# Kernel tuning notes

Hardware: AMD Instinct MI355X
Metric: run time of the kernel (lower is better)

Reference implementation:

```python
import jax, jax.numpy as jnp
import numpy as np
import math

B, S, D = 4, 1024, 1024
H, DK, DV = 16, 64, 64
MAX_REL = 32  # use_neg_dist=True -> vocab = 2*MAX_REL+1


def setup_inputs() -> dict:
    key = jax.random.key(0)
    ks = jax.random.split(key, 13)
    sc = 0.02
    return {
        "key": jax.random.normal(ks[0], (B, S, D), jnp.float32),
        "value": jax.random.normal(ks[1], (B, S, D), jnp.float32),
        "query": jax.random.normal(ks[2], (B, S, D), jnp.float32),
        "Wk": jax.random.normal(ks[3], (D, H * DK), jnp.float32) * sc,
        "bk": jnp.zeros((H * DK,), jnp.float32),
        "Wq": jax.random.normal(ks[4], (D, H * DK), jnp.float32) * sc,
        "bq": jnp.zeros((H * DK,), jnp.float32),
        "Wv": jax.random.normal(ks[5], (D, H * DV), jnp.float32) * sc,
        "bv": jnp.zeros((H * DV,), jnp.float32),
        "Wo": jax.random.normal(ks[6], (H * DV, D), jnp.float32) * sc,
        "bo": jnp.zeros((D,), jnp.float32),
        "emb_k": jax.random.normal(ks[7], (2 * MAX_REL + 1, DK), jnp.float32) * sc,
        "emb_v": jax.random.normal(ks[8], (2 * MAX_REL + 1, DV), jnp.float32) * sc,
    }


def reference(key, value, query, Wk, bk, Wq, bq, Wv, bv, Wo, bo, emb_k, emb_v):
    # project and split heads -> [B, H, S, d]
    def shape(x, d):
        return x.reshape(B, S, H, d).transpose(0, 2, 1, 3)

    k = shape(key @ Wk + bk, DK)
    v = shape(value @ Wv + bv, DV)
    q = shape(query @ Wq + bq, DK)

    # relative position ids: [S, S] in [0, 2*MAX_REL]
    r = jnp.arange(S)
    rel_idx = jnp.clip(r[None, :] - r[:, None], -MAX_REL, MAX_REL) + MAX_REL
    rel_k = emb_k[rel_idx]  # [S, S, DK]
    rel_v = emb_v[rel_idx]  # [S, S, DV]

    q = q / math.sqrt(DK)
    # content scores + relative-key scores (relative_matmul with transpose=True)
    scores = jnp.einsum("bhqd,bhkd->bhqk", q, k) + jnp.einsum("bhqd,qkd->bhqk", q, rel_k)
    attn = jax.nn.softmax(scores.astype(jnp.float32), axis=-1).astype(q.dtype)

    # context + relative-value contribution (relative_matmul with transpose=False)
    ctx = jnp.einsum("bhqk,bhkd->bhqd", attn, v) + jnp.einsum("bhqk,qkd->bhqd", attn, rel_v)
    ctx = ctx.transpose(0, 2, 1, 3).reshape(B, S, H * DV)
    final_output = ctx @ Wo + bo
    return final_output, attn
```

## Files before the change

### kernel.cpp

```cpp
#include <hip/hip_runtime.h>
#include <hip/hip_bf16.h>

#define B_ 4
#define S_ 1024
#define D_ 1024
#define H_ 16

typedef unsigned short u16;
typedef __bf16 bf16x8 __attribute__((ext_vector_type(8)));
typedef float f32x4 __attribute__((ext_vector_type(4)));

__device__ inline u16 f2bf(float f) {
    __bf16 h = (__bf16)f;
    return __builtin_bit_cast(u16, h);
}
__device__ inline float bf2f(u16 u) {
    unsigned int x = ((unsigned int)u) << 16;
    return __builtin_bit_cast(float, x);
}
__device__ inline void gl_lds16(const u16* g, u16* lbase) {
    __builtin_amdgcn_global_load_lds(
        (const __attribute__((address_space(1))) unsigned int*)g,
        (__attribute__((address_space(3))) unsigned int*)lbase, 16, 0, 0);
}
__device__ inline bf16x8 frag_swz(const u16* lds, int row, int chunk) {
    int off = (row << 6) + ((chunk ^ (row & 7)) << 3);
    return *(const bf16x8*)(lds + off);
}
__device__ inline bf16x8 frag_p(const u16* lds, int row, int chunk) {
    int off = row * 72 + (chunk << 3);
    return *(const bf16x8*)(lds + off);
}
__device__ inline f32x4 mfma16(bf16x8 a, bf16x8 b, f32x4 c) {
    return __builtin_amdgcn_mfma_f32_16x16x32_bf16(a, b, c, 0, 0, 0);
}
__device__ inline void bar() {
    asm volatile("s_waitcnt lgkmcnt(0)\n\ts_barrier" ::: "memory");
}
__device__ inline void wait_vm0() {
    asm volatile("s_waitcnt vmcnt(0)" ::: "memory");
    __builtin_amdgcn_sched_barrier(0);
}
__device__ inline void wait_vm2() {
    asm volatile("s_waitcnt vmcnt(2)" ::: "memory");
    __builtin_amdgcn_sched_barrier(0);
}
__device__ inline void wait_lgkm0() {
    asm volatile("s_waitcnt lgkmcnt(0)" ::: "memory");
    __builtin_amdgcn_sched_barrier(0);
}

__global__ __launch_bounds__(256) void cast_bf16_kernel(const float* __restrict__ src,
                                                        u16* __restrict__ dst, int n) {
    int i = (blockIdx.x * 256 + threadIdx.x) * 4;
    if (i >= n) return;
    float4 v = *(const float4*)(src + i);
    ushort4 o;
    o.x = f2bf(v.x); o.y = f2bf(v.y); o.z = f2bf(v.z); o.w = f2bf(v.w);
    *(ushort4*)(dst + i) = o;
}

__global__ __launch_bounds__(256) void tcast_kernel(const float* __restrict__ src,
                                                    u16* __restrict__ dst) {
    __shared__ float tile[32][33];
    int bx = blockIdx.x, by = blockIdx.y;
    int tx = threadIdx.x, ty = threadIdx.y;
    int x = bx * 32 + tx;
    for (int i = ty; i < 32; i += 8)
        tile[i][tx] = src[(size_t)(by * 32 + i) * 1024 + x];
    __syncthreads();
    int col = by * 32 + tx;
    for (int i = ty; i < 32; i += 8)
        dst[(size_t)(bx * 32 + i) * 1024 + col] = f2bf(tile[tx][i]);
}

__device__ inline void gemm_core(const u16* __restrict__ A, const u16* __restrict__ Bt,
                                 int m0, int n0, u16* lsA, u16* lsB, f32x4 acc[4][4]) {
    int tid = threadIdx.x, lane = tid & 63, wave = tid >> 6;
    int quad = lane >> 4, l16 = lane & 15;
    int wm = wave >> 1, wn = wave & 1;
    f32x4 z = {0.0f, 0.0f, 0.0f, 0.0f};
    for (int mi = 0; mi < 4; mi++)
        for (int ni = 0; ni < 4; ni++) acc[mi][ni] = z;
    for (int k0 = 0; k0 < 1024; k0 += 64) {
        const u16* abase = A + (size_t)m0 * 1024 + k0;
        const u16* bbase = Bt + (size_t)n0 * 1024 + k0;
        for (int j = 0; j < 4; j++) {
            int C = (wave * 4 + j) * 64 + lane;
            int row = C >> 3, c = C & 7;
            int sw = (c ^ (row & 7)) << 3;
            gl_lds16(abase + (size_t)row * 1024 + sw, lsA + (wave * 4 + j) * 512);
            gl_lds16(bbase + (size_t)row * 1024 + sw, lsB + (wave * 4 + j) * 512);
        }
        __syncthreads();
        for (int s = 0; s < 2; s++) {
            bf16x8 af[4], bfv[4];
            for (int mi = 0; mi < 4; mi++) af[mi] = frag_swz(lsA, wm * 64 + mi * 16 + l16, s * 4 + quad);
            for (int ni = 0; ni < 4; ni++) bfv[ni] = frag_swz(lsB, wn * 64 + ni * 16 + l16, s * 4 + quad);
            for (int mi = 0; mi < 4; mi++)
                for (int ni = 0; ni < 4; ni++)
                    acc[mi][ni] = mfma16(af[mi], bfv[ni], acc[mi][ni]);
        }
        __syncthreads();
    }
}

__global__ __launch_bounds__(256) void gemm_proj_kernel(
    const u16* __restrict__ xq, const u16* __restrict__ xk, const u16* __restrict__ xv,
    const u16* __restrict__ wt,
    const float* __restrict__ bq, const float* __restrict__ bk, const float* __restrict__ bv,
    u16* __restrict__ qb, u16* __restrict__ kb, u16* __restrict__ vtb) {
    __shared__ __align__(16) u16 lsA[128 * 64];
    __shared__ __align__(16) u16 lsB[128 * 64];
    int bid = blockIdx.x;
    int which = bid >> 8;
    int t = bid & 255;
    int m0 = (t >> 3) * 128, n0 = (t & 7) * 128;
    const u16* A = which == 0 ? xq : (which == 1 ? xk : xv);
    const u16* Bt = wt + (size_t)which * 1024 * 1024;
    const float* bias = which == 0 ? bq : (which == 1 ? bk : bv);
    f32x4 acc[4][4];
    gemm_core(A, Bt, m0, n0, lsA, lsB, acc);
    int tid = threadIdx.x, lane = tid & 63, wave = tid >> 6;
    int quad = lane >> 4, l16 = lane & 15;
    int wm = wave >> 1, wn = wave & 1;
    for (int mi = 0; mi < 4; mi++) {
        int rbase = m0 + wm * 64 + mi * 16 + quad * 4;
        int b = rbase >> 10, s0 = rbase & 1023;
        for (int ni = 0; ni < 4; ni++) {
            int n = n0 + wn * 64 + ni * 16 + l16;
            int h = n >> 6, d = n & 63;
            float bsv = bias[n];
            if (which == 2) {
                ushort4 pk;
                pk.x = f2bf(acc[mi][ni][0] + bsv);
                pk.y = f2bf(acc[mi][ni][1] + bsv);
                pk.z = f2bf(acc[mi][ni][2] + bsv);
                pk.w = f2bf(acc[mi][ni][3] + bsv);
                *(ushort4*)(vtb + ((size_t)(b * H_ + h) * 64 + d) * 1024 + s0) = pk;
            } else {
                u16* outp = (which == 0) ? qb : kb;
                float scl = (which == 0) ? 0.125f : 1.0f;
                for (int r = 0; r < 4; r++) {
                    int s = s0 + r;
                    outp[((size_t)(b * H_ + h) * 1024 + s) * 64 + d] = f2bf((acc[mi][ni][r] + bsv) * scl);
                }
            }
        }
    }
}

__global__ __launch_bounds__(256) void gemm_final_kernel(const u16* __restrict__ ctxb,
                                                         const u16* __restrict__ wot,
                                                         const float* __restrict__ bo,
                                                         float* __restrict__ out) {
    __shared__ __align__(16) u16 lsA[128 * 64];
    __shared__ __align__(16) u16 lsB[128 * 64];
    int bid = blockIdx.x;
    int m0 = (bid >> 3) * 128, n0 = (bid & 7) * 128;
    f32x4 acc[4][4];
    gemm_core(ctxb, wot, m0, n0, lsA, lsB, acc);
    int tid = threadIdx.x, lane = tid & 63, wave = tid >> 6;
    int quad = lane >> 4, l16 = lane & 15;
    int wm = wave >> 1, wn = wave & 1;
    for (int mi = 0; mi < 4; mi++)
        for (int ni = 0; ni < 4; ni++) {
            int n = n0 + wn * 64 + ni * 16 + l16;
            float bsv = bo[n];
            for (int r = 0; r < 4; r++) {
                int row = m0 + wm * 64 + mi * 16 + quad * 4 + r;
                out[(size_t)row * 1024 + n] = acc[mi][ni][r] + bsv;
            }
        }
}

__global__ __launch_bounds__(256, 3) void attn_kernel(
    const u16* __restrict__ qb, const u16* __restrict__ kb, const u16* __restrict__ vtb,
    const float* __restrict__ emb_k, const float* __restrict__ emb_v,
    float* __restrict__ attn_out, u16* __restrict__ ctxb) {
    __shared__ __align__(16) u16 kbuf[2][64 * 64];
    __shared__ __align__(16) u16 pbuf[64 * 72];
    __shared__ __align__(16) u16 wqbuf[64 * 72];
    __shared__ __align__(16) u16 qrel[64 * 68];

    int bid = blockIdx.x;
    int qt = bid & 15, bh = bid >> 4;
    int tid = threadIdx.x, lane = tid & 63, wave = tid >> 6;
    int quad = lane >> 4, l16 = lane & 15;
    int mrow = wave * 16;

    const u16* qbase = qb + ((size_t)bh * 1024 + qt * 64) * 64;
    const u16* kbh = kb + (size_t)bh * 1024 * 64;
    const u16* vbh = vtb + (size_t)bh * 64 * 1024;

    auto stage = [&](const u16* src, int srcStride, u16* dst) {
#pragma unroll
        for (int j = 0; j < 2; j++) {
            int C = (wave * 2 + j) * 64 + lane;
            int row = C >> 3, c = C & 7;
            gl_lds16(src + (size_t)row * srcStride + ((c ^ (row & 7)) << 3),
                     dst + (wave * 2 + j) * 512);
        }
    };

    stage(qbase, 64, wqbuf);
    for (int i = tid; i < 65 * 64; i += 256) {
        int j = i >> 6, d = i & 63;
        pbuf[(j << 6) + ((((d >> 3) ^ (j & 7)) << 3) | (d & 7))] = f2bf(emb_k[i]);
    }
    wait_vm0();
    bar();

    {
        bf16x8 a0 = frag_swz(wqbuf, mrow + l16, quad);
        bf16x8 a1 = frag_swz(wqbuf, mrow + l16, 4 + quad);
#pragma unroll
        for (int ni = 0; ni < 5; ni++) {
            int rr = ni * 16 + l16;
            rr = rr > 64 ? 64 : rr;
            f32x4 a = {0.0f, 0.0f, 0.0f, 0.0f};
            a = mfma16(a0, frag_swz(pbuf, rr, quad), a);
            a = mfma16(a1, frag_swz(pbuf, rr, 4 + quad), a);
            int j = ni * 16 + l16;
            if (j < 65) {
#pragma unroll
                for (int r = 0; r < 4; r++)
                    qrel[(mrow + quad * 4 + r) * 68 + j] = f2bf(a[r]);
            }
        }
    }
    bf16x8 aq0 = frag_swz(wqbuf, mrow + l16, quad);
    bf16x8 aq1 = frag_swz(wqbuf, mrow + l16, 4 + quad);
    stage(kbh, 64, kbuf[0]);
    bar();

    {
        unsigned int* wz = (unsigned int*)wqbuf;
        for (int i = lane; i < 16 * 36; i += 64) wz[mrow * 36 + i] = 0u;
    }

    float m_run[4] = {-1e30f, -1e30f, -1e30f, -1e30f};
    float l_run[4] = {0.0f, 0.0f, 0.0f, 0.0f};

#pragma unroll 1
    for (int kt = 0; kt < 16; kt++) {
        if (kt < 15) {
            stage(kbh + (size_t)(kt + 1) * 4096, 64, kbuf[(kt + 1) & 1]);
            wait_vm2();
        } else {
            wait_vm0();
        }
        bar();
        const u16* kl = kbuf[kt & 1];
        f32x4 sc[4];
#pragma unroll
        for (int ni = 0; ni < 4; ni++) {
            f32x4 a = {0.0f, 0.0f, 0.0f, 0.0f};
            a = mfma16(aq0, frag_swz(kl, ni * 16 + l16, quad), a);
            a = mfma16(aq1, frag_swz(kl, ni * 16 + l16, 4 + quad), a);
            sc[ni] = a;
        }
        float s[4][4];
#pragma unroll
        for (int ni = 0; ni < 4; ni++)
#pragma unroll
            for (int r = 0; r < 4; r++) {
                int ql = mrow + quad * 4 + r;
                int qg = qt * 64 + ql;
                int kg = kt * 64 + ni * 16 + l16;
                int jj = kg - qg;
                jj = jj < -32 ? -32 : (jj > 32 ? 32 : jj);
                s[ni][r] = sc[ni][r] + bf2f(qrel[ql * 68 + jj + 32]);
            }
#pragma unroll
        for (int r = 0; r < 4; r++) {
            float mx = fmaxf(fmaxf(s[0][r], s[1][r]), fmaxf(s[2][r], s[3][r]));
            mx = fmaxf(mx, __shfl_xor(mx, 1));
            mx = fmaxf(mx, __shfl_xor(mx, 2));
            mx = fmaxf(mx, __shfl_xor(mx, 4));
            mx = fmaxf(mx, __shfl_xor(mx, 8));
            float mnew = fmaxf(m_run[r], mx);
            float su = __expf(s[0][r] - mnew) + __expf(s[1][r] - mnew) +
                       __expf(s[2][r] - mnew) + __expf(s[3][r] - mnew);
            su += __shfl_xor(su, 1);
            su += __shfl_xor(su, 2);
            su += __shfl_xor(su, 4);
            su += __shfl_xor(su, 8);
            l_run[r] = l_run[r] * __expf(m_run[r] - mnew) + su;
            m_run[r] = mnew;
        }
        bar();
    }

    float rl[4];
#pragma unroll
    for (int r = 0; r < 4; r++) rl[r] = 1.0f / l_run[r];
    float wl[4] = {0.0f, 0.0f, 0.0f, 0.0f};
    float wr[4] = {0.0f, 0.0f, 0.0f, 0.0f};
    f32x4 ctx[4];
    {
        f32x4 z = {0.0f, 0.0f, 0.0f, 0.0f};
#pragma unroll
        for (int ni = 0; ni < 4; ni++) ctx[ni] = z;
    }
    float* attn_bh = attn_out + (size_t)bh * 1024 * 1024;

#pragma unroll 1
    for (int kt = 0; kt < 16; kt++) {
        stage(kbh + (size_t)kt * 4096, 64, kbuf[0]);
        stage(vbh + kt * 64, 1024, kbuf[1]);
        wait_vm0();
        bar();
        f32x4 sc[4];
#pragma unroll
        for (int ni = 0; ni < 4; ni++) {
            f32x4 a = {0.0f, 0.0f, 0.0f, 0.0f};
            a = mfma16(aq0, frag_swz(kbuf[0], ni * 16 + l16, quad), a);
            a = mfma16(aq1, frag_swz(kbuf[0], ni * 16 + l16, 4 + quad), a);
            sc[ni] = a;
        }
#pragma unroll
        for (int ni = 0; ni < 4; ni++)
#pragma unroll
            for (int r = 0; r < 4; r++) {
                int ql = mrow + quad * 4 + r;
                int qg = qt * 64 + ql;
                int kg = kt * 64 + ni * 16 + l16;
                int jj = kg - qg;
                int jc = jj < -32 ? -32 : (jj > 32 ? 32 : jj);
                float s = sc[ni][r] + bf2f(qrel[ql * 68 + jc + 32]);
                float p = __expf(s - m_run[r]) * rl[r];
                __builtin_nontemporal_store(p, &attn_bh[(size_t)qg * 1024 + kg]);
                u16 pb = f2bf(p);
                pbuf[ql * 72 + ni * 16 + l16] = pb;
                if (jj <= -32) wl[r] += p;
                else if (jj >= 32) wr[r] += p;
                else wqbuf[ql * 72 + jj + 32] = pb;
            }
        wait_lgkm0();
#pragma unroll
        for (int s2 = 0; s2 < 2; s2++) {
            bf16x8 af = frag_p(pbuf, mrow + l16, s2 * 4 + quad);
#pragma unroll
            for (int ni = 0; ni < 4; ni++)
                ctx[ni] = mfma16(af, frag_swz(kbuf[1], ni * 16 + l16, s2 * 4 + quad), ctx[ni]);
        }
        bar();
    }

#pragma unroll
    for (int r = 0; r < 4; r++) {
        wl[r] += __shfl_xor(wl[r], 1); wl[r] += __shfl_xor(wl[r], 2);
        wl[r] += __shfl_xor(wl[r], 4); wl[r] += __shfl_xor(wl[r], 8);
        wr[r] += __shfl_xor(wr[r], 1); wr[r] += __shfl_xor(wr[r], 2);
        wr[r] += __shfl_xor(wr[r], 4); wr[r] += __shfl_xor(wr[r], 8);
    }
    if (l16 == 0) {
#pragma unroll
        for (int r = 0; r < 4; r++)
            wqbuf[(mrow + quad * 4 + r) * 72] = f2bf(wl[r]);
    }
    u16* evt = kbuf[0];
    for (int i = tid; i < 4096; i += 256) {
        int j = i >> 6, d = i & 63;
        evt[d * 72 + j] = f2bf(emb_v[i]);
    }
    __syncthreads();
#pragma unroll
    for (int s2 = 0; s2 < 2; s2++) {
        bf16x8 af = frag_p(wqbuf, mrow + l16, s2 * 4 + quad);
#pragma unroll
        for (int ni = 0; ni < 4; ni++)
            ctx[ni] = mfma16(af, frag_p(evt, ni * 16 + l16, s2 * 4 + quad), ctx[ni]);
    }
#pragma unroll
    for (int ni = 0; ni < 4; ni++) {
        float ev = emb_v[64 * 64 + ni * 16 + l16];
#pragma unroll
        for (int r = 0; r < 4; r++) ctx[ni][r] += wr[r] * ev;
    }

    int b = bh >> 4, h = bh & 15;
#pragma unroll
    for (int ni = 0; ni < 4; ni++)
#pragma unroll
        for (int r = 0; r < 4; r++) {
            int ql = mrow + quad * 4 + r;
            int sg = qt * 64 + ql;
            ctxb[((size_t)b * 1024 + sg) * 1024 + h * 64 + ni * 16 + l16] = f2bf(ctx[ni][r]);
        }
}

extern "C" void kernel_launch(void* const* d_in, const int* in_sizes, int n_in,
                              void* d_out, int out_size, void* d_ws, size_t ws_size,
                              hipStream_t stream) {
    const float* key_f   = (const float*)d_in[0];
    const float* value_f = (const float*)d_in[1];
    const float* query_f = (const float*)d_in[2];
    const float* Wk = (const float*)d_in[3];
    const float* bk = (const float*)d_in[4];
    const float* Wq = (const float*)d_in[5];
    const float* bq = (const float*)d_in[6];
    const float* Wv = (const float*)d_in[7];
    const float* bv = (const float*)d_in[8];
    const float* Wo = (const float*)d_in[9];
    const float* bo = (const float*)d_in[10];
    const float* emb_k = (const float*)d_in[11];
    const float* emb_v = (const float*)d_in[12];

    char* ws = (char*)d_ws;
    const size_t MB = 1024 * 1024;
    u16* xq   = (u16*)(ws + 0 * MB);
    u16* xk   = (u16*)(ws + 8 * MB);
    u16* xv   = (u16*)(ws + 16 * MB);
    u16* wt   = (u16*)(ws + 24 * MB);
    u16* wot  = (u16*)(ws + 30 * MB);
    u16* qb   = (u16*)(ws + 32 * MB);
    u16* kb   = (u16*)(ws + 40 * MB);
    u16* vtb  = (u16*)(ws + 48 * MB);
    u16* ctxb = (u16*)(ws + 56 * MB);

    float* out0 = (float*)d_out;
    float* attn = out0 + (size_t)4 * 1024 * 1024;

    cast_bf16_kernel<<<4096, 256, 0, stream>>>(query_f, xq, 4194304);
    cast_bf16_kernel<<<4096, 256, 0, stream>>>(key_f,   xk, 4194304);
    cast_bf16_kernel<<<4096, 256, 0, stream>>>(value_f, xv, 4194304);
    dim3 tg(32, 32), tb(32, 8);
    tcast_kernel<<<tg, tb, 0, stream>>>(Wq, wt);
    tcast_kernel<<<tg, tb, 0, stream>>>(Wk, wt + 1024 * 1024);
    tcast_kernel<<<tg, tb, 0, stream>>>(Wv, wt + 2 * 1024 * 1024);
    tcast_kernel<<<tg, tb, 0, stream>>>(Wo, wot);
    gemm_proj_kernel<<<768, 256, 0, stream>>>(xq, xk, xv, wt, bq, bk, bv, qb, kb, vtb);
    attn_kernel<<<1024, 256, 0, stream>>>(qb, kb, vtb, emb_k, emb_v, attn, ctxb);
    gemm_final_kernel<<<256, 256, 0, stream>>>(ctxb, wot, bo, out0);
}
```

Before: 548.5 us.

## Shrink attention LDS buffers with XOR swizzle to fit four blocks per CU

New measurement: 558.2 us. No clear change (+1.8%).

```diff
diff --git a/kernel.cpp b/kernel.cpp
--- a/kernel.cpp
+++ b/kernel.cpp
@@ -27,9 +27,8 @@
     int off = (row << 6) + ((chunk ^ (row & 7)) << 3);
     return *(const bf16x8*)(lds + off);
 }
-__device__ inline bf16x8 frag_p(const u16* lds, int row, int chunk) {
-    int off = row * 72 + (chunk << 3);
-    return *(const bf16x8*)(lds + off);
+__device__ inline int swz_idx(int row, int col) {
+    return (row << 6) + ((((col >> 3) ^ (row & 7)) << 3) | (col & 7));
 }
 __device__ inline f32x4 mfma16(bf16x8 a, bf16x8 b, f32x4 c) {
     return __builtin_amdgcn_mfma_f32_16x16x32_bf16(a, b, c, 0, 0, 0);
@@ -174,14 +173,14 @@
         }
 }
 
-__global__ __launch_bounds__(256, 3) void attn_kernel(
+__global__ __launch_bounds__(256, 4) void attn_kernel(
     const u16* __restrict__ qb, const u16* __restrict__ kb, const u16* __restrict__ vtb,
     const float* __restrict__ emb_k, const float* __restrict__ emb_v,
     float* __restrict__ attn_out, u16* __restrict__ ctxb) {
     __shared__ __align__(16) u16 kbuf[2][64 * 64];
-    __shared__ __align__(16) u16 pbuf[64 * 72];
-    __shared__ __align__(16) u16 wqbuf[64 * 72];
-    __shared__ __align__(16) u16 qrel[64 * 68];
+    __shared__ __align__(16) u16 pbuf[64 * 64];
+    __shared__ __align__(16) u16 wqbuf[64 * 64];
+    __shared__ __align__(16) u16 qrel[64 * 64];
 
     int bid = blockIdx.x;
     int qt = bid & 15, bh = bid >> 4;
@@ -206,37 +205,43 @@
     stage(qbase, 64, wqbuf);
     for (int i = tid; i < 65 * 64; i += 256) {
         int j = i >> 6, d = i & 63;
-        pbuf[(j << 6) + ((((d >> 3) ^ (j & 7)) << 3) | (d & 7))] = f2bf(emb_k[i]);
+        u16 v = f2bf(emb_k[i]);
+        if (j < 64) pbuf[swz_idx(j, d)] = v;
+        else kbuf[0][d] = v;
     }
     wait_vm0();
     bar();
 
+    float q64[4];
     {
         bf16x8 a0 = frag_swz(wqbuf, mrow + l16, quad);
         bf16x8 a1 = frag_swz(wqbuf, mrow + l16, 4 + quad);
 #pragma unroll
-        for (int ni = 0; ni < 5; ni++) {
-            int rr = ni * 16 + l16;
-            rr = rr > 64 ? 64 : rr;
+        for (int ni = 0; ni < 4; ni++) {
             f32x4 a = {0.0f, 0.0f, 0.0f, 0.0f};
-            a = mfma16(a0, frag_swz(pbuf, rr, quad), a);
-            a = mfma16(a1, frag_swz(pbuf, rr, 4 + quad), a);
-            int j = ni * 16 + l16;
-            if (j < 65) {
-#pragma unroll
-                for (int r = 0; r < 4; r++)
-                    qrel[(mrow + quad * 4 + r) * 68 + j] = f2bf(a[r]);
-            }
+            a = mfma16(a0, frag_swz(pbuf, ni * 16 + l16, quad), a);
+            a = mfma16(a1, frag_swz(pbuf, ni * 16 + l16, 4 + quad), a);
+#pragma unroll
+            for (int r = 0; r < 4; r++)
+                qrel[(mrow + quad * 4 + r) * 64 + ni * 16 + l16] = f2bf(a[r]);
+        }
+        {
+            f32x4 a = {0.0f, 0.0f, 0.0f, 0.0f};
+            a = mfma16(a0, frag_swz(kbuf[0], 0, quad), a);
+            a = mfma16(a1, frag_swz(kbuf[0], 0, 4 + quad), a);
+#pragma unroll
+            for (int r = 0; r < 4; r++) q64[r] = a[r];
         }
     }
     bf16x8 aq0 = frag_swz(wqbuf, mrow + l16, quad);
     bf16x8 aq1 = frag_swz(wqbuf, mrow + l16, 4 + quad);
+    wait_lgkm0();
+    bar();
+
     stage(kbh, 64, kbuf[0]);
-    bar();
-
     {
         unsigned int* wz = (unsigned int*)wqbuf;
-        for (int i = lane; i < 16 * 36; i += 64) wz[mrow * 36 + i] = 0u;
+        for (int i = lane; i < 16 * 32; i += 64) wz[mrow * 32 + i] = 0u;
     }
 
     float m_run[4] = {-1e30f, -1e30f, -1e30f, -1e30f};
@@ -269,8 +274,9 @@
                 int qg = qt * 64 + ql;
                 int kg = kt * 64 + ni * 16 + l16;
                 int jj = kg - qg;
-                jj = jj < -32 ? -32 : (jj > 32 ? 32 : jj);
-                s[ni][r] = sc[ni][r] + bf2f(qrel[ql * 68 + jj + 32]);
+                float rel = (jj >= 32) ? q64[r]
+                          : bf2f(qrel[(ql << 6) + (jj < -32 ? 0 : jj + 32)]);
+                s[ni][r] = sc[ni][r] + rel;
             }
 #pragma unroll
         for (int r = 0; r < 4; r++) {
@@ -327,20 +333,21 @@
                 int qg = qt * 64 + ql;
                 int kg = kt * 64 + ni * 16 + l16;
                 int jj = kg - qg;
-                int jc = jj < -32 ? -32 : (jj > 32 ? 32 : jj);
-                float s = sc[ni][r] + bf2f(qrel[ql * 68 + jc + 32]);
+                float rel = (jj >= 32) ? q64[r]
+                          : bf2f(qrel[(ql << 6) + (jj < -32 ? 0 : jj + 32)]);
+                float s = sc[ni][r] + rel;
                 float p = __expf(s - m_run[r]) * rl[r];
                 __builtin_nontemporal_store(p, &attn_bh[(size_t)qg * 1024 + kg]);
                 u16 pb = f2bf(p);
-                pbuf[ql * 72 + ni * 16 + l16] = pb;
+                pbuf[swz_idx(ql, ni * 16 + l16)] = pb;
                 if (jj <= -32) wl[r] += p;
                 else if (jj >= 32) wr[r] += p;
-                else wqbuf[ql * 72 + jj + 32] = pb;
+                else wqbuf[swz_idx(ql, jj + 32)] = pb;
             }
         wait_lgkm0();
 #pragma unroll
         for (int s2 = 0; s2 < 2; s2++) {
-            bf16x8 af = frag_p(pbuf, mrow + l16, s2 * 4 + quad);
+            bf16x8 af = frag_swz(pbuf, mrow + l16, s2 * 4 + quad);
 #pragma unroll
             for (int ni = 0; ni < 4; ni++)
                 ctx[ni] = mfma16(af, frag_swz(kbuf[1], ni * 16 + l16, s2 * 4 + quad), ctx[ni]);
@@ -357,21 +364,23 @@
     }
     if (l16 == 0) {
 #pragma unroll
-        for (int r = 0; r < 4; r++)
-            wqbuf[(mrow + quad * 4 + r) * 72] = f2bf(wl[r]);
+        for (int r = 0; r < 4; r++) {
+            int q = mrow + quad * 4 + r;
+            wqbuf[swz_idx(q, 0)] = f2bf(wl[r]);
+        }
     }
     u16* evt = kbuf[0];
     for (int i = tid; i < 4096; i += 256) {
         int j = i >> 6, d = i & 63;
-        evt[d * 72 + j] = f2bf(emb_v[i]);
+        evt[swz_idx(d, j)] = f2bf(emb_v[i]);
     }
     __syncthreads();
 #pragma unroll
     for (int s2 = 0; s2 < 2; s2++) {
-        bf16x8 af = frag_p(wqbuf, mrow + l16, s2 * 4 + quad);
+        bf16x8 af = frag_swz(wqbuf, mrow + l16, s2 * 4 + quad);
 #pragma unroll
         for (int ni = 0; ni < 4; ni++)
-            ctx[ni] = mfma16(af, frag_p(evt, ni * 16 + l16, s2 * 4 + quad), ctx[ni]);
+            ctx[ni] = mfma16(af, frag_swz(evt, ni * 16 + l16, s2 * 4 + quad), ctx[ni]);
     }
 #pragma unroll
     for (int ni = 0; ni < 4; ni++) {
```

## Double-buffer K and V tiles in the attention output pass

Applied to the files above, without the earlier changes.

Result: no change. 549.0 us (+0.1%).

```diff
diff --git a/kernel.cpp b/kernel.cpp
--- a/kernel.cpp
+++ b/kernel.cpp
@@ -43,6 +43,18 @@
 }
 __device__ inline void wait_vm2() {
     asm volatile("s_waitcnt vmcnt(2)" ::: "memory");
+    __builtin_amdgcn_sched_barrier(0);
+}
+__device__ inline void wait_vm4() {
+    asm volatile("s_waitcnt vmcnt(4)" ::: "memory");
+    __builtin_amdgcn_sched_barrier(0);
+}
+__device__ inline void wait_vm16() {
+    asm volatile("s_waitcnt vmcnt(16)" ::: "memory");
+    __builtin_amdgcn_sched_barrier(0);
+}
+__device__ inline void wait_vm20() {
+    asm volatile("s_waitcnt vmcnt(20)" ::: "memory");
     __builtin_amdgcn_sched_barrier(0);
 }
 __device__ inline void wait_lgkm0() {
@@ -174,11 +186,11 @@
         }
 }
 
-__global__ __launch_bounds__(256, 3) void attn_kernel(
+__global__ __launch_bounds__(256, 2) void attn_kernel(
     const u16* __restrict__ qb, const u16* __restrict__ kb, const u16* __restrict__ vtb,
     const float* __restrict__ emb_k, const float* __restrict__ emb_v,
     float* __restrict__ attn_out, u16* __restrict__ ctxb) {
-    __shared__ __align__(16) u16 kbuf[2][64 * 64];
+    __shared__ __align__(16) u16 kv[2][2][64 * 64];
     __shared__ __align__(16) u16 pbuf[64 * 72];
     __shared__ __align__(16) u16 wqbuf[64 * 72];
     __shared__ __align__(16) u16 qrel[64 * 68];
@@ -231,7 +243,7 @@
     }
     bf16x8 aq0 = frag_swz(wqbuf, mrow + l16, quad);
     bf16x8 aq1 = frag_swz(wqbuf, mrow + l16, 4 + quad);
-    stage(kbh, 64, kbuf[0]);
+    stage(kbh, 64, kv[0][0]);
     bar();
 
     {
@@ -245,13 +257,13 @@
 #pragma unroll 1
     for (int kt = 0; kt < 16; kt++) {
         if (kt < 15) {
-            stage(kbh + (size_t)(kt + 1) * 4096, 64, kbuf[(kt + 1) & 1]);
+            stage(kbh + (size_t)(kt + 1) * 4096, 64, kv[0][(kt + 1) & 1]);
             wait_vm2();
         } else {
             wait_vm0();
         }
         bar();
-        const u16* kl = kbuf[kt & 1];
+        const u16* kl = kv[0][kt & 1];
         f32x4 sc[4];
 #pragma unroll
         for (int ni = 0; ni < 4; ni++) {
@@ -305,18 +317,28 @@
     }
     float* attn_bh = attn_out + (size_t)bh * 1024 * 1024;
 
+    stage(kbh, 64, kv[0][0]);
+    stage(vbh, 1024, kv[1][0]);
+    wait_vm0();
+    bar();
 #pragma unroll 1
     for (int kt = 0; kt < 16; kt++) {
-        stage(kbh + (size_t)kt * 4096, 64, kbuf[0]);
-        stage(vbh + kt * 64, 1024, kbuf[1]);
-        wait_vm0();
+        if (kt < 15) {
+            stage(kbh + (size_t)(kt + 1) * 4096, 64, kv[0][(kt + 1) & 1]);
+            stage(vbh + (kt + 1) * 64, 1024, kv[1][(kt + 1) & 1]);
+        }
+        if (kt == 0) wait_vm4();
+        else if (kt == 15) wait_vm16();
+        else wait_vm20();
         bar();
+        const u16* kl = kv[0][kt & 1];
+        const u16* vl = kv[1][kt & 1];
         f32x4 sc[4];
 #pragma unroll
         for (int ni = 0; ni < 4; ni++) {
             f32x4 a = {0.0f, 0.0f, 0.0f, 0.0f};
-            a = mfma16(aq0, frag_swz(kbuf[0], ni * 16 + l16, quad), a);
-            a = mfma16(aq1, frag_swz(kbuf[0], ni * 16 + l16, 4 + quad), a);
+            a = mfma16(aq0, frag_swz(kl, ni * 16 + l16, quad), a);
+            a = mfma16(aq1, frag_swz(kl, ni * 16 + l16, 4 + quad), a);
             sc[ni] = a;
         }
 #pragma unroll
@@ -343,7 +365,7 @@
             bf16x8 af = frag_p(pbuf, mrow + l16, s2 * 4 + quad);
 #pragma unroll
             for (int ni = 0; ni < 4; ni++)
-                ctx[ni] = mfma16(af, frag_swz(kbuf[1], ni * 16 + l16, s2 * 4 + quad), ctx[ni]);
+                ctx[ni] = mfma16(af, frag_swz(vl, ni * 16 + l16, s2 * 4 + quad), ctx[ni]);
         }
         bar();
     }
@@ -360,7 +382,7 @@
         for (int r = 0; r < 4; r++)
             wqbuf[(mrow + quad * 4 + r) * 72] = f2bf(wl[r]);
     }
-    u16* evt = kbuf[0];
+    u16* evt = kv[0][0];
     for (int i = tid; i < 4096; i += 256) {
         int j = i >> 6, d = i & 63;
         evt[d * 72 + j] = f2bf(emb_v[i]);
```
